# Optimization experiments

Hardware: AMD Instinct MI355X
Metric: run time of the kernel (lower is better)

Reference implementation:

```python
import jax, jax.numpy as jnp
import numpy as np

H, KD, VD, KNN = 8, 64, 64, 128
D, FC, N, S = 512, 2048, 4, 1024
GW_DEC, GW_ENC = 0.5, 0.5
EPS = 1e-5
SCALE = float(np.sqrt(KD))


def _layer_norm(x):
    # nn.LayerNorm(out_dim, eps=1e-5, elementwise_affine=False)
    m = jnp.mean(x, -1, keepdims=True)
    v = jnp.var(x, -1, keepdims=True)
    return (x - m) * jax.lax.rsqrt(v + EPS)


def _mha(x, Wk, bk, Wv, bv, Wo, bo, att_graph, gw, mask, Wq=None, bq=None, q_in=None):
    # x: [N,S,D]; per-head projections stacked: Wk [H,D,Kd], Wv [H,D,Vd]
    key = jnp.einsum('nsd,hdk->hnsk', x, Wk) + bk[:, None, None, :]
    value = jnp.einsum('nsd,hdv->hnsv', x, Wv) + bv[:, None, None, :]
    if q_in is None:
        query = key  # self-attention: query = key (as in the torch code)
    else:
        query = jnp.einsum('nqd,hdk->hnqk', q_in, Wq) + bq[:, None, None, :]
    # broadcast-mul-sum in torch == batched matmul
    att = jnp.einsum('hnqk,hnsk->hnqs', query, key) / SCALE  # [H,N,Q,S]
    if mask:
        qlen, slen = att.shape[-2], att.shape[-1]
        causal = jnp.arange(slen)[None, :] <= jnp.arange(qlen)[:, None]
        att = jnp.where(causal, att, -jnp.inf)
    # knn sparsification: keep top-KNN per row, rest -> -inf (equiv to topk+scatter for distinct values)
    thresh = jax.lax.top_k(att, KNN)[0][..., -1:]
    att = jnp.where(att >= thresh, att, -jnp.inf)
    att = jax.nn.softmax(att, axis=-1)
    # blend with precomputed (softmaxed) graph attention
    att = gw * att_graph + (1.0 - gw) * att
    ctx = jnp.einsum('hnqs,hnsv->hnqv', att, value)  # [H,N,Q,Vd]
    ctx = jnp.transpose(ctx, (1, 2, 0, 3)).reshape(ctx.shape[1], ctx.shape[2], H * VD)
    return ctx @ Wo + bo


def setup_inputs() -> dict:
    key = jax.random.key(0)
    ks = jax.random.split(key, 22)
    p = lambda k, shp: (0.02 * jax.random.normal(k, shp)).astype(jnp.float32)
    return {
        'z': jax.random.normal(ks[0], (N, S, D), jnp.float32),
        'y': jax.random.normal(ks[1], (N, S, D), jnp.float32),
        'graph_dec': jax.random.normal(ks[2], (S, S), jnp.float32),
        'graph_enc': jax.random.normal(ks[3], (S, S), jnp.float32),
        'dec_Wk': p(ks[4], (H, D, KD)), 'dec_bk': p(ks[5], (H, KD)),
        'dec_Wv': p(ks[6], (H, D, VD)), 'dec_bv': p(ks[7], (H, VD)),
        'dec_Wo': p(ks[8], (H * VD, D)), 'dec_bo': p(ks[9], (D,)),
        'enc_Wk': p(ks[10], (H, D, KD)), 'enc_bk': p(ks[11], (H, KD)),
        'enc_Wq': p(ks[12], (H, D, KD)), 'enc_bq': p(ks[13], (H, KD)),
        'enc_Wv': p(ks[14], (H, D, VD)), 'enc_bv': p(ks[15], (H, VD)),
        'enc_Wo': p(ks[16], (H * VD, D)), 'enc_bo': p(ks[17], (D,)),
        'fc_W1': p(ks[18], (D, FC)), 'fc_b1': p(ks[19], (FC,)),
        'fc_W2': p(ks[20], (FC, D)), 'fc_b2': p(ks[21], (D,)),
    }


def reference(z, y, graph_dec, graph_enc, dec_Wk, dec_bk, dec_Wv, dec_bv, dec_Wo, dec_bo, enc_Wk, enc_bk, enc_Wq, enc_bq, enc_Wv, enc_bv, enc_Wo, enc_bo, fc_W1, fc_b1, fc_W2, fc_b2):
    # graphs are row-softmaxed at construction time in the torch module
    gdec = jax.nn.softmax(graph_dec, axis=-1)
    genc = jax.nn.softmax(graph_enc, axis=-1)
    # 1) masked decoder self-attention on y
    h = _mha(y, dec_Wk, dec_bk, dec_Wv, dec_bv, dec_Wo, dec_bo, gdec, GW_DEC, True)
    h = _layer_norm(h + y)
    # 2) encoder-decoder attention: keys/values from z, query from h via query_keys (query_key=True)
    h2 = _mha(z, enc_Wk, enc_bk, enc_Wv, enc_bv, enc_Wo, enc_bo, genc, GW_ENC, False, enc_Wq, enc_bq, h)
    h2 = _layer_norm(h2 + h)
    # 3) two-layer MLP
    h3 = jax.nn.relu(h2 @ fc_W1 + fc_b1) @ fc_W2 + fc_b2
    return _layer_norm(h3 + h2)
```

## Files before the change

kernel.cpp:

```cpp
#include <hip/hip_runtime.h>
#include <stdint.h>

typedef short short8 __attribute__((ext_vector_type(8)));
typedef short short4v __attribute__((ext_vector_type(4)));
typedef float floatx4 __attribute__((ext_vector_type(4)));
typedef unsigned uint4v __attribute__((ext_vector_type(4)));

#define H_  8
#define NB_ 4
#define S_  1024
#define D_  512
#define KD_ 64

__device__ __forceinline__ short f2bf(float f){
    unsigned u = __builtin_bit_cast(unsigned, f);
    u += 0x7fffu + ((u>>16)&1u);
    return (short)(u>>16);
}
__device__ __forceinline__ float wred_addf(float x){
    #pragma unroll
    for(int o=32;o>0;o>>=1) x += __shfl_xor(x,o,64);
    return x;
}
__device__ __forceinline__ float wred_maxf(float x){
    #pragma unroll
    for(int o=32;o>0;o>>=1) x = fmaxf(x,__shfl_xor(x,o,64));
    return x;
}
__device__ __forceinline__ unsigned umaxu(unsigned a, unsigned b){ return a>b?a:b; }
__device__ __forceinline__ unsigned uminu(unsigned a, unsigned b){ return a<b?a:b; }

template<int CTRL, int RMASK, int BC>
__device__ __forceinline__ unsigned dppu(unsigned x){
    return (unsigned)__builtin_amdgcn_update_dpp(0, (int)x, CTRL, RMASK, 0xf, BC);
}
template<int CTRL, int RMASK>
__device__ __forceinline__ unsigned dppu_m1(unsigned x){
    return (unsigned)__builtin_amdgcn_update_dpp((int)0xFFFFFFFF, (int)x, CTRL, RMASK, 0xf, 0);
}
__device__ __forceinline__ unsigned wsum_dpp_u(unsigned x){
    x += dppu<0x111,0xf,1>(x);
    x += dppu<0x112,0xf,1>(x);
    x += dppu<0x114,0xf,1>(x);
    x += dppu<0x118,0xf,1>(x);
    x += dppu<0x142,0xa,0>(x);
    x += dppu<0x143,0xc,0>(x);
    return (unsigned)__builtin_amdgcn_readlane((int)x, 63);
}
__device__ __forceinline__ unsigned wmax_dpp_u(unsigned x){
    x = umaxu(x, dppu<0x111,0xf,1>(x));
    x = umaxu(x, dppu<0x112,0xf,1>(x));
    x = umaxu(x, dppu<0x114,0xf,1>(x));
    x = umaxu(x, dppu<0x118,0xf,1>(x));
    x = umaxu(x, dppu<0x142,0xa,0>(x));
    x = umaxu(x, dppu<0x143,0xc,0>(x));
    return (unsigned)__builtin_amdgcn_readlane((int)x, 63);
}
__device__ __forceinline__ unsigned wmin_dpp_u(unsigned x){
    x = uminu(x, dppu_m1<0x111,0xf>(x));
    x = uminu(x, dppu_m1<0x112,0xf>(x));
    x = uminu(x, dppu_m1<0x114,0xf>(x));
    x = uminu(x, dppu_m1<0x118,0xf>(x));
    x = uminu(x, dppu_m1<0x142,0xa>(x));
    x = uminu(x, dppu_m1<0x143,0xc>(x));
    return (unsigned)__builtin_amdgcn_readlane((int)x, 63);
}
__device__ __forceinline__ float addu_f(float a, unsigned b){
    return a + __builtin_bit_cast(float, b);
}
__device__ __forceinline__ float wsum_dpp_f(float x){
    x = addu_f(x, dppu<0x111,0xf,1>(__builtin_bit_cast(unsigned,x)));
    x = addu_f(x, dppu<0x112,0xf,1>(__builtin_bit_cast(unsigned,x)));
    x = addu_f(x, dppu<0x114,0xf,1>(__builtin_bit_cast(unsigned,x)));
    x = addu_f(x, dppu<0x118,0xf,1>(__builtin_bit_cast(unsigned,x)));
    x = addu_f(x, dppu<0x142,0xa,0>(__builtin_bit_cast(unsigned,x)));
    x = addu_f(x, dppu<0x143,0xc,0>(__builtin_bit_cast(unsigned,x)));
    return __builtin_bit_cast(float, (unsigned)__builtin_amdgcn_readlane((int)__builtin_bit_cast(unsigned, x), 63));
}
__device__ __forceinline__ unsigned cvt_pk_bf16(float a, float b){
    unsigned r;
    asm("v_cvt_pk_bf16_f32 %0, %1, %2" : "=v"(r) : "v"(a), "v"(b));
    return r;
}
__device__ __forceinline__ unsigned count128(const unsigned (&kv)[16], unsigned mid){
    unsigned cv = 0u;
    #pragma unroll
    for(int j=0;j<8;j++) cv += (unsigned)(kv[j] >= mid);
    unsigned cs = 0u;
    #pragma unroll
    for(int j=8;j<16;j++) cs += (unsigned)__popcll(__ballot(kv[j] >= mid));
    return wsum_dpp_u(cv) + cs;
}

__global__ __launch_bounds__(256) void cvt2_kernel(const float* __restrict__ a, const float* __restrict__ b,
                                                   short* __restrict__ oa, short* __restrict__ ob){
    const float* in = blockIdx.y ? b : a;
    short* out = blockIdx.y ? ob : oa;
    int i = (blockIdx.x*256 + threadIdx.x)*4;
    floatx4 v = *(const floatx4*)(in + i);
    short4v r;
    #pragma unroll
    for(int j=0;j<4;j++) r[j] = f2bf(v[j]);
    *(short4v*)(out + i) = r;
}

__global__ __launch_bounds__(256) void wtrans5_kernel(
    const float* __restrict__ dWk, const float* __restrict__ dWv,
    const float* __restrict__ eWk, const float* __restrict__ eWv, const float* __restrict__ eWq,
    short* __restrict__ wKVd, short* __restrict__ wKVe, short* __restrict__ wQet)
{
    __shared__ float t[32][33];
    int zz = blockIdx.z; int w = zz>>3, h = zz&7;
    const float* src; short* dst;
    if(w==0){ src = dWk + h*32768; dst = wKVd + h*65536; }
    else if(w==1){ src = dWv + h*32768; dst = wKVd + h*65536 + 32768; }
    else if(w==2){ src = eWk + h*32768; dst = wKVe + h*65536; }
    else if(w==3){ src = eWv + h*32768; dst = wKVe + h*65536 + 32768; }
    else { src = eWq + h*32768; dst = wQet + h*32768; }
    const int R = 512, C = 64;
    int c0 = blockIdx.x*32, r0 = blockIdx.y*32;
    int tid = threadIdx.x;
    int r = tid>>3, cq = (tid&7)*4;
    #pragma unroll
    for(int i=0;i<4;i++) t[r][cq+i] = src[(r0+r)*C + c0+cq+i];
    __syncthreads();
    int c = tid>>3, rq = (tid&7)*4;
    #pragma unroll
    for(int i=0;i<4;i++) dst[(c0+c)*R + r0+rq+i] = f2bf(t[rq+i][c]);
}

__global__ __launch_bounds__(256) void wtrans4_kernel(
    const float* __restrict__ dWo, const float* __restrict__ eWo,
    const float* __restrict__ W1, const float* __restrict__ W2,
    short* __restrict__ oWod, short* __restrict__ oWoe,
    short* __restrict__ oW1, short* __restrict__ oW2)
{
    __shared__ float t[32][33];
    int id = blockIdx.x;
    const float* src; short* dst; int R, C, c0, r0;
    if(id < 512){
        src = (id<256)? dWo : eWo; dst = (id<256)? oWod : oWoe;
        int tt = id & 255; R = 512; C = 512;
        c0 = (tt&15)*32; r0 = (tt>>4)*32;
    } else if(id < 1536){
        src = W1; dst = oW1; int tt = id - 512; R = 512; C = 2048;
        c0 = (tt&63)*32; r0 = (tt>>6)*32;
    } else {
        src = W2; dst = oW2; int tt = id - 1536; R = 2048; C = 512;
        c0 = (tt&15)*32; r0 = (tt>>4)*32;
    }
    int tid = threadIdx.x;
    int r = tid>>3, cq = (tid&7)*4;
    #pragma unroll
    for(int i=0;i<4;i++) t[r][cq+i] = src[(long)(r0+r)*C + c0+cq+i];
    __syncthreads();
    int c = tid>>3, rq = (tid&7)*4;
    #pragma unroll
    for(int i=0;i<4;i++) dst[(long)(c0+c)*R + r0+rq+i] = f2bf(t[rq+i][c]);
}

__global__ __launch_bounds__(256) void graph_softmax_kernel(const float* __restrict__ g0,
                                                            const float* __restrict__ g1,
                                                            short* __restrict__ o0,
                                                            short* __restrict__ o1){
    int row = blockIdx.x;
    const float* g = blockIdx.y ? g1 : g0;
    short* o = blockIdx.y ? o1 : o0;
    const float* gr = g + (long)row*S_;
    short* orow = o + (long)row*S_;
    int tid = threadIdx.x, wave = tid>>6, lane = tid&63;
    __shared__ float red[8];
    float v[4]; float mx = -3.0e38f;
    #pragma unroll
    for(int i=0;i<4;i++){ v[i] = gr[tid + 256*i]; mx = fmaxf(mx, v[i]); }
    mx = wred_maxf(mx);
    if(lane==0) red[wave] = mx;
    __syncthreads();
    mx = fmaxf(fmaxf(red[0],red[1]), fmaxf(red[2],red[3]));
    float s = 0.f;
    #pragma unroll
    for(int i=0;i<4;i++){ v[i] = __expf(v[i]-mx); s += v[i]; }
    s = wred_addf(s);
    if(lane==0) red[4+wave] = s;
    __syncthreads();
    s = red[4]+red[5]+red[6]+red[7];
    float inv = 0.5f/s;
    #pragma unroll
    for(int i=0;i<4;i++) orow[tid + 256*i] = f2bf(v[i]*inv);
}

template<int KV>
__global__ __launch_bounds__(256) void gemm_proj_kernel(
    const short* __restrict__ A, const short* __restrict__ Bt,
    const float* __restrict__ b1, const float* __restrict__ b2,
    short* __restrict__ o1, short* __restrict__ o2)
{
    constexpr int TN = KV ? 128 : 64;
    constexpr int NI = TN/32;
    __shared__ short As[64*32];
    __shared__ short Bs[TN*32];
    int z = blockIdx.z;
    int m0 = blockIdx.x*64;
    const short* Bb = Bt + (long)z*(TN*512);
    int tid = threadIdx.x, wave = tid>>6, lane = tid&63, quad = lane>>4, nl = lane&15;
    int wm = (wave&1)*32, wn = (wave>>1)*(TN/2);
    floatx4 acc[2][NI];
    #pragma unroll
    for(int i=0;i<2;i++)
        #pragma unroll
        for(int j=0;j<NI;j++) acc[i][j] = (floatx4){0.f,0.f,0.f,0.f};
    int r = tid>>2, c = (tid&3)*8;
    for(int k0=0;k0<512;k0+=32){
        __syncthreads();
        __builtin_amdgcn_global_load_lds(
            (const __attribute__((address_space(1))) unsigned*)(A + (long)(m0 + r)*512 + k0 + c),
            (__attribute__((address_space(3))) unsigned*)((char*)As + wave*1024), 16, 0, 0);
        #pragma unroll
        for(int i=0;i<TN/64;i++)
            __builtin_amdgcn_global_load_lds(
                (const __attribute__((address_space(1))) unsigned*)(Bb + (long)(r + i*64)*512 + k0 + c),
                (__attribute__((address_space(3))) unsigned*)((char*)Bs + i*4096 + wave*1024), 16, 0, 0);
        __syncthreads();
        short8 af[2], bfr[NI];
        #pragma unroll
        for(int i=0;i<2;i++) af[i] = *(const short8*)(As + (wm + i*16 + nl)*32 + quad*8);
        #pragma unroll
        for(int j=0;j<NI;j++) bfr[j] = *(const short8*)(Bs + (wn + j*16 + nl)*32 + quad*8);
        #pragma unroll
        for(int i=0;i<2;i++)
            #pragma unroll
            for(int j=0;j<NI;j++)
                acc[i][j] = __builtin_amdgcn_mfma_f32_16x16x32_bf16(af[i],bfr[j],acc[i][j],0,0,0);
    }
    #pragma unroll
    for(int j=0;j<NI;j++){
        int n = wn + j*16 + nl;
        float bv = (KV && n >= 64) ? b2[z*64 + n - 64] : b1[z*64 + n];
        #pragma unroll
        for(int i=0;i<2;i++){
            #pragma unroll
            for(int rr=0;rr<4;rr++){
                int m = m0 + wm + i*16 + quad*4 + rr;
                float v = acc[i][j][rr] + bv;
                long zb = (long)(z*NB_ + (m>>10));
                if(KV && n >= 64) o2[ (zb*KD_ + (n-64))*S_ + (m&1023) ] = f2bf(v);
                else              o1[ (zb*S_ + (m&1023))*KD_ + n ] = f2bf(v);
            }
        }
    }
}

template<int TM, int TN, int OUTBF, int RELU>
__global__ __launch_bounds__(256) void gemm_big_kernel(
    const short* __restrict__ A, const short* __restrict__ Bt, const float* __restrict__ bias,
    void* __restrict__ out, int M, int N, int K)
{
    __shared__ short As[TM*32];
    __shared__ short Bs[TN*32];
    int m0 = blockIdx.x*TM, n0 = blockIdx.y*TN;
    int tid = threadIdx.x, wave = tid>>6, lane = tid&63, quad = lane>>4, nl = lane&15;
    constexpr int MI = TM/32, NI = TN/32;
    int wm = (wave&1)*(TM/2), wn = (wave>>1)*(TN/2);
    floatx4 acc[MI][NI];
    #pragma unroll
    for(int i=0;i<MI;i++)
        #pragma unroll
        for(int j=0;j<NI;j++) acc[i][j] = (floatx4){0.f,0.f,0.f,0.f};

    int r = tid>>2, c = (tid&3)*8;
    for(int k0=0;k0<K;k0+=32){
        __syncthreads();
        #pragma unroll
        for(int i=0;i<TM/64;i++)
            __builtin_amdgcn_global_load_lds(
                (const __attribute__((address_space(1))) unsigned*)(A + (long)(m0 + r + i*64)*K + k0 + c),
                (__attribute__((address_space(3))) unsigned*)((char*)As + i*4096 + wave*1024),
                16, 0, 0);
        #pragma unroll
        for(int i=0;i<TN/64;i++)
            __builtin_amdgcn_global_load_lds(
                (const __attribute__((address_space(1))) unsigned*)(Bt + (long)(n0 + r + i*64)*K + k0 + c),
                (__attribute__((address_space(3))) unsigned*)((char*)Bs + i*4096 + wave*1024),
                16, 0, 0);
        __syncthreads();
        short8 af[MI], bfr[NI];
        #pragma unroll
        for(int i=0;i<MI;i++) af[i] = *(const short8*)(As + (wm + i*16 + nl)*32 + quad*8);
        #pragma unroll
        for(int j=0;j<NI;j++) bfr[j] = *(const short8*)(Bs + (wn + j*16 + nl)*32 + quad*8);
        #pragma unroll
        for(int i=0;i<MI;i++)
            #pragma unroll
            for(int j=0;j<NI;j++)
                acc[i][j] = __builtin_amdgcn_mfma_f32_16x16x32_bf16(af[i],bfr[j],acc[i][j],0,0,0);
    }
    #pragma unroll
    for(int j=0;j<NI;j++){
        int n = n0 + wn + j*16 + nl;
        float bv = bias[n];
        #pragma unroll
        for(int i=0;i<MI;i++){
            #pragma unroll
            for(int rr=0;rr<4;rr++){
                int m = m0 + wm + i*16 + quad*4 + rr;
                float v = acc[i][j][rr] + bv;
                if(RELU) v = fmaxf(v, 0.f);
                if(OUTBF) ((short*)out)[(long)m*N + n] = f2bf(v);
                else      ((float*)out)[(long)m*N + n] = v;
            }
        }
    }
}

__global__ __launch_bounds__(512,6) void attn_kernel(
    const short* __restrict__ Qb, const short* __restrict__ Kb, const short* __restrict__ Vt,
    const short* __restrict__ graph, short* __restrict__ ctx, int causal)
{
    __shared__ short attb[16*1024];
    __shared__ float pbuf[16*68];
    int hn = blockIdx.x, qt = blockIdx.y;
    int h = hn>>2, n = hn&3;
    int q0 = qt*16;
    int tid=threadIdx.x, wave=tid>>6, lane=tid&63, quad=lane>>4, nl=lane&15;

    if(causal){
        uint4v fv = (uint4v){0xff80ff80u,0xff80ff80u,0xff80ff80u,0xff80ff80u};
        #pragma unroll
        for(int i=0;i<4;i++) *(uint4v*)((char*)attb + tid*16 + i*8192) = fv;
        __syncthreads();
    }

    const short* Qp = Qb + ((long)hn*S_ + q0 + nl)*KD_ + quad*8;
    short8 aq0 = *(const short8*)(Qp);
    short8 aq1 = *(const short8*)(Qp + 32);
    const short* Kp = Kb + (long)hn*S_*KD_;
    int stmax = causal ? qt : 63;
    for(int st=wave; st<=stmax; st+=8){
        const short* kp = Kp + (st*16 + nl)*KD_ + quad*8;
        short8 b0 = *(const short8*)(kp);
        short8 b1 = *(const short8*)(kp + 32);
        floatx4 cc = (floatx4){0.f,0.f,0.f,0.f};
        cc = __builtin_amdgcn_mfma_f32_16x16x32_bf16(aq0,b0,cc,0,0,0);
        cc = __builtin_amdgcn_mfma_f32_16x16x32_bf16(aq1,b1,cc,0,0,0);
        int s = st*16 + nl;
        #pragma unroll
        for(int rr=0;rr<4;rr++){
            int q = quad*4 + rr;
            short val = f2bf(cc[rr]*0.125f);
            if(causal && s > q0 + q) val = (short)0xff80;
            attb[q*1024 + ((s + 8*q)&1023)] = val;
        }
    }
    __syncthreads();

    #pragma unroll 1
    for(int rp=0; rp<2; ++rp){
        int q = wave*2 + rp;
        int qg = q0 + q;
        short* rowp = attb + q*1024;
        int sb = lane*16;
        int p0 = (sb + 8*q) & 1023;
        const short* grow = graph + (long)qg*1024 + sb;
        uint4v g0 = *(const uint4v*)(grow);
        uint4v g1 = *(const uint4v*)(grow + 8);
        uint4v u0 = *(const uint4v*)(rowp + p0);
        uint4v u1 = *(const uint4v*)(rowp + ((p0+8)&1023));
        unsigned pr[8];
        #pragma unroll
        for(int i=0;i<4;i++){ pr[i] = u0[i]; pr[4+i] = u1[i]; }
        unsigned kv[16];
        #pragma unroll
        for(int i=0;i<8;i++){
            unsigned u = pr[i];
            unsigned kp = u ^ (0x80008000u + ((u>>15)&0x00010001u)*0x7fffu);
            kv[2*i]   = kp & 0xffffu;
            kv[2*i+1] = kp >> 16;
        }
        unsigned a0 = umaxu(kv[0],kv[1]),  a1 = umaxu(kv[2],kv[3]);
        unsigned a2 = umaxu(kv[4],kv[5]),  a3 = umaxu(kv[6],kv[7]);
        unsigned a4 = umaxu(kv[8],kv[9]),  a5 = umaxu(kv[10],kv[11]);
        unsigned a6 = umaxu(kv[12],kv[13]),a7 = umaxu(kv[14],kv[15]);
        unsigned mk = umaxu(umaxu(umaxu(a0,a1),umaxu(a2,a3)), umaxu(umaxu(a4,a5),umaxu(a6,a7)));
        unsigned mks = wmax_dpp_u(mk);
        unsigned lmin = wmin_dpp_u(mk);
        unsigned lo, hi;
        {
            unsigned cnt = count128(kv, lmin);
            if(cnt >= 128u){ lo = lmin; hi = (cnt == 128u) ? (lmin + 1u) : (mks + 1u); }
            else           { lo = 0u;   hi = lmin; }
        }
        while(hi - lo > 1u){
            unsigned mid = (lo + hi) >> 1;
            unsigned cnt = count128(kv, mid);
            if(cnt >= 128u){ lo = mid; if(cnt == 128u) break; }
            else hi = mid;
        }
        unsigned uo = (mks & 0x8000u) ? ((mks & 0x7fffu)<<16) : ((~mks)<<16);
        float mxf = __builtin_bit_cast(float, uo);
        float ev[16]; float sm = 0.f;
        #pragma unroll
        for(int i=0;i<8;i++){
            float f0 = __builtin_bit_cast(float, pr[i] << 16);
            float f1 = __builtin_bit_cast(float, pr[i] & 0xffff0000u);
            float e0 = __expf(f0 - mxf);
            float e1 = __expf(f1 - mxf);
            e0 = (kv[2*i]   >= lo) ? e0 : 0.f;
            e1 = (kv[2*i+1] >= lo) ? e1 : 0.f;
            ev[2*i] = e0; ev[2*i+1] = e1;
            sm += e0 + e1;
        }
        sm = wsum_dpp_f(sm);
        float inv = 0.5f / sm;
        uint4v w0, w1;
        #pragma unroll
        for(int i=0;i<4;i++){
            float gl0 = __builtin_bit_cast(float, g0[i] << 16);
            float gh0 = __builtin_bit_cast(float, g0[i] & 0xffff0000u);
            w0[i] = cvt_pk_bf16(fmaf(ev[2*i], inv, gl0), fmaf(ev[2*i+1], inv, gh0));
            float gl1 = __builtin_bit_cast(float, g1[i] << 16);
            float gh1 = __builtin_bit_cast(float, g1[i] & 0xffff0000u);
            w1[i] = cvt_pk_bf16(fmaf(ev[8+2*i], inv, gl1), fmaf(ev[8+2*i+1], inv, gh1));
        }
        *(uint4v*)(rowp + p0) = w0;
        *(uint4v*)(rowp + ((p0+8)&1023)) = w1;
    }
    __syncthreads();

    int vh = wave & 3, sh = wave >> 2;
    int v0 = vh*16;
    const short* Vp = Vt + ((long)hn*KD_ + v0 + nl)*S_;
    floatx4 o4 = (floatx4){0.f,0.f,0.f,0.f};
    int arow = nl;
    int sbase = sh*512;
    for(int s0=sbase; s0<sbase+512; s0+=32){
        int cs = (s0 + quad*8 + 8*arow) & 1023;
        short8 ap = *(const short8*)(attb + arow*1024 + cs);
        short8 bv = *(const short8*)(Vp + s0 + quad*8);
        o4 = __builtin_amdgcn_mfma_f32_16x16x32_bf16(ap,bv,o4,0,0,0);
    }
    if(sh==1){
        #pragma unroll
        for(int rr=0;rr<4;rr++) pbuf[(quad*4+rr)*68 + v0 + nl] = o4[rr];
    }
    __syncthreads();
    if(sh==0){
        #pragma unroll
        for(int rr=0;rr<4;rr++){
            int q = quad*4 + rr;
            float v = o4[rr] + pbuf[q*68 + v0 + nl];
            ctx[ ((long)(n*S_ + q0 + q))*512 + h*KD_ + v0 + nl ] = f2bf(v);
        }
    }
}

__global__ __launch_bounds__(256) void ln_kernel(const float* __restrict__ x, const float* __restrict__ res,
                                                 float* __restrict__ outf, short* __restrict__ outb){
    long row = blockIdx.x;
    const float* xr = x + row*D_;
    const float* rr = res + row*D_;
    int tid = threadIdx.x, wave = tid>>6, lane = tid&63;
    float t0 = xr[tid] + rr[tid];
    float t1 = xr[tid+256] + rr[tid+256];
    float s = t0 + t1, s2 = t0*t0 + t1*t1;
    __shared__ float red[8];
    s = wred_addf(s); s2 = wred_addf(s2);
    if(lane==0){ red[wave] = s; red[4+wave] = s2; }
    __syncthreads();
    s  = red[0]+red[1]+red[2]+red[3];
    s2 = red[4]+red[5]+red[6]+red[7];
    float mean = s*(1.f/512.f);
    float var = s2*(1.f/512.f) - mean*mean;
    float rs = rsqrtf(var + 1e-5f);
    float o0 = (t0-mean)*rs, o1 = (t1-mean)*rs;
    if(outf){ outf[row*D_+tid] = o0; outf[row*D_+tid+256] = o1; }
    if(outb){ outb[row*D_+tid] = f2bf(o0); outb[row*D_+tid+256] = f2bf(o1); }
}

extern "C" void kernel_launch(void* const* d_in, const int* in_sizes, int n_in,
                              void* d_out, int out_size, void* d_ws, size_t ws_size,
                              hipStream_t stream)
{
    const float* z         = (const float*)d_in[0];
    const float* y         = (const float*)d_in[1];
    const float* graph_dec = (const float*)d_in[2];
    const float* graph_enc = (const float*)d_in[3];
    const float* dec_Wk = (const float*)d_in[4];  const float* dec_bk = (const float*)d_in[5];
    const float* dec_Wv = (const float*)d_in[6];  const float* dec_bv = (const float*)d_in[7];
    const float* dec_Wo = (const float*)d_in[8];  const float* dec_bo = (const float*)d_in[9];
    const float* enc_Wk = (const float*)d_in[10]; const float* enc_bk = (const float*)d_in[11];
    const float* enc_Wq = (const float*)d_in[12]; const float* enc_bq = (const float*)d_in[13];
    const float* enc_Wv = (const float*)d_in[14]; const float* enc_bv = (const float*)d_in[15];
    const float* enc_Wo = (const float*)d_in[16]; const float* enc_bo = (const float*)d_in[17];
    const float* fc_W1  = (const float*)d_in[18]; const float* fc_b1  = (const float*)d_in[19];
    const float* fc_W2  = (const float*)d_in[20]; const float* fc_b2  = (const float*)d_in[21];

    char* ws = (char*)d_ws;
    short* gdec  = (short*)(ws + 0x0000000);
    short* genc  = (short*)(ws + 0x0400000);
    short* y_bf  = (short*)(ws + 0x0800000);
    short* z_bf  = (short*)(ws + 0x0C00000);
    short* Kdec  = (short*)(ws + 0x1000000);
    short* Vtdec = (short*)(ws + 0x1400000);
    short* Kenc  = (short*)(ws + 0x1800000);
    short* Vtenc = (short*)(ws + 0x1C00000);
    short* Qenc  = (short*)(ws + 0x2000000);
    short* ctx   = (short*)(ws + 0x2400000);
    float* tmp   = (float*)(ws + 0x2800000);
    float* hbuf  = (float*)(ws + 0x3000000);
    short* h_bf  = (short*)(ws + 0x3800000);
    float* h2    = (float*)(ws + 0x3C00000);
    short* h2_bf = (short*)(ws + 0x4400000);
    short* fc1   = (short*)(ws + 0x4800000);
    short* wKVd  = (short*)(ws + 0x5800000);
    short* wKVe  = (short*)(ws + 0x5900000);
    short* wQet  = (short*)(ws + 0x5A00000);
    short* wOdt  = (short*)(ws + 0x5A80000);
    short* wOet  = (short*)(ws + 0x5B00000);
    short* wF1t  = (short*)(ws + 0x5B80000);
    short* wF2t  = (short*)(ws + 0x5D80000);
    float* outp  = (float*)d_out;

    dim3 B(256);
    wtrans5_kernel<<<dim3(2,16,40),B,0,stream>>>(dec_Wk, dec_Wv, enc_Wk, enc_Wv, enc_Wq, wKVd, wKVe, wQet);
    wtrans4_kernel<<<dim3(2560),B,0,stream>>>(dec_Wo, enc_Wo, fc_W1, fc_W2, wOdt, wOet, wF1t, wF2t);
    cvt2_kernel<<<dim3(2048,2),B,0,stream>>>(y, z, y_bf, z_bf);
    graph_softmax_kernel<<<dim3(1024,2),B,0,stream>>>(graph_dec, graph_enc, gdec, genc);
    gemm_proj_kernel<1><<<dim3(64,1,8),B,0,stream>>>(y_bf, wKVd, dec_bk, dec_bv, Kdec, Vtdec);
    attn_kernel<<<dim3(32,64),dim3(512),0,stream>>>(Kdec, Kdec, Vtdec, gdec, ctx, 1);
    gemm_big_kernel<64,128,0,0><<<dim3(64,4),B,0,stream>>>(ctx, wOdt, dec_bo, tmp, 4096, 512, 512);
    ln_kernel<<<dim3(4096),B,0,stream>>>(tmp, y, hbuf, h_bf);
    gemm_proj_kernel<1><<<dim3(64,1,8),B,0,stream>>>(z_bf, wKVe, enc_bk, enc_bv, Kenc, Vtenc);
    gemm_proj_kernel<0><<<dim3(64,1,8),B,0,stream>>>(h_bf, wQet, enc_bq, (const float*)0, Qenc, (short*)0);
    attn_kernel<<<dim3(32,64),dim3(512),0,stream>>>(Qenc, Kenc, Vtenc, genc, ctx, 0);
    gemm_big_kernel<64,128,0,0><<<dim3(64,4),B,0,stream>>>(ctx, wOet, enc_bo, tmp, 4096, 512, 512);
    ln_kernel<<<dim3(4096),B,0,stream>>>(tmp, hbuf, h2, h2_bf);
    gemm_big_kernel<128,128,1,1><<<dim3(32,16),B,0,stream>>>(h2_bf, wF1t, fc_b1, fc1, 4096, 2048, 512);
    gemm_big_kernel<64,128,0,0><<<dim3(64,4),B,0,stream>>>(fc1, wF2t, fc_b2, tmp, 4096, 512, 2048);
    ln_kernel<<<dim3(4096),B,0,stream>>>(tmp, h2, outp, (short*)0);
}
```

Measured before the change: 387.9 us.

## Fuse prep kernels, merge KV projections, fuse output GEMMs with LayerNorm, interpolate top-k search

Folds the four preprocessing kernels into one prep kernel and merges the decoder and encoder K/V projections into a single launch. The three output-projection GEMMs now do bias, residual add and LayerNorm inside one 16-row by 512-column tile per block, which drops the fp32 tmp buffer and the separate ln_kernel launches. The top-k threshold search in attention now alternates interpolation steps with bisection steps to need fewer count iterations. The trade-off is that the fused GEMM+LN uses small 16-row tiles with 1024 threads and only 256 blocks, so it reuses each B tile less and may run below full occupancy.

```diff
diff --git a/kernel.cpp b/kernel.cpp
--- a/kernel.cpp
+++ b/kernel.cpp
@@ -92,123 +92,125 @@
     return wsum_dpp_u(cv) + cs;
 }
 
-__global__ __launch_bounds__(256) void cvt2_kernel(const float* __restrict__ a, const float* __restrict__ b,
-                                                   short* __restrict__ oa, short* __restrict__ ob){
-    const float* in = blockIdx.y ? b : a;
-    short* out = blockIdx.y ? ob : oa;
-    int i = (blockIdx.x*256 + threadIdx.x)*4;
-    floatx4 v = *(const floatx4*)(in + i);
-    short4v r;
-    #pragma unroll
-    for(int j=0;j<4;j++) r[j] = f2bf(v[j]);
-    *(short4v*)(out + i) = r;
-}
-
-__global__ __launch_bounds__(256) void wtrans5_kernel(
+__global__ __launch_bounds__(256) void prep_kernel(
     const float* __restrict__ dWk, const float* __restrict__ dWv,
     const float* __restrict__ eWk, const float* __restrict__ eWv, const float* __restrict__ eWq,
-    short* __restrict__ wKVd, short* __restrict__ wKVe, short* __restrict__ wQet)
-{
-    __shared__ float t[32][33];
-    int zz = blockIdx.z; int w = zz>>3, h = zz&7;
-    const float* src; short* dst;
-    if(w==0){ src = dWk + h*32768; dst = wKVd + h*65536; }
-    else if(w==1){ src = dWv + h*32768; dst = wKVd + h*65536 + 32768; }
-    else if(w==2){ src = eWk + h*32768; dst = wKVe + h*65536; }
-    else if(w==3){ src = eWv + h*32768; dst = wKVe + h*65536 + 32768; }
-    else { src = eWq + h*32768; dst = wQet + h*32768; }
-    const int R = 512, C = 64;
-    int c0 = blockIdx.x*32, r0 = blockIdx.y*32;
-    int tid = threadIdx.x;
-    int r = tid>>3, cq = (tid&7)*4;
-    #pragma unroll
-    for(int i=0;i<4;i++) t[r][cq+i] = src[(r0+r)*C + c0+cq+i];
-    __syncthreads();
-    int c = tid>>3, rq = (tid&7)*4;
-    #pragma unroll
-    for(int i=0;i<4;i++) dst[(c0+c)*R + r0+rq+i] = f2bf(t[rq+i][c]);
-}
-
-__global__ __launch_bounds__(256) void wtrans4_kernel(
     const float* __restrict__ dWo, const float* __restrict__ eWo,
     const float* __restrict__ W1, const float* __restrict__ W2,
+    const float* __restrict__ y, const float* __restrict__ z,
+    const float* __restrict__ g0, const float* __restrict__ g1,
+    short* __restrict__ wKVd, short* __restrict__ wKVe, short* __restrict__ wQet,
     short* __restrict__ oWod, short* __restrict__ oWoe,
-    short* __restrict__ oW1, short* __restrict__ oW2)
+    short* __restrict__ oW1, short* __restrict__ oW2,
+    short* __restrict__ y_bf, short* __restrict__ z_bf,
+    short* __restrict__ og0, short* __restrict__ og1)
 {
     __shared__ float t[32][33];
     int id = blockIdx.x;
-    const float* src; short* dst; int R, C, c0, r0;
-    if(id < 512){
-        src = (id<256)? dWo : eWo; dst = (id<256)? oWod : oWoe;
-        int tt = id & 255; R = 512; C = 512;
-        c0 = (tt&15)*32; r0 = (tt>>4)*32;
-    } else if(id < 1536){
-        src = W1; dst = oW1; int tt = id - 512; R = 512; C = 2048;
-        c0 = (tt&63)*32; r0 = (tt>>6)*32;
+    int tid = threadIdx.x;
+    if(id < 1280){
+        int zz = id >> 5; int rem = id & 31; int by = rem >> 1, bx = rem & 1;
+        int w = zz>>3, h = zz&7;
+        const float* src; short* dst;
+        if(w==0){ src = dWk + h*32768; dst = wKVd + h*65536; }
+        else if(w==1){ src = dWv + h*32768; dst = wKVd + h*65536 + 32768; }
+        else if(w==2){ src = eWk + h*32768; dst = wKVe + h*65536; }
+        else if(w==3){ src = eWv + h*32768; dst = wKVe + h*65536 + 32768; }
+        else { src = eWq + h*32768; dst = wQet + h*32768; }
+        int c0 = bx*32, r0 = by*32;
+        int r = tid>>3, cq = (tid&7)*4;
+        #pragma unroll
+        for(int i=0;i<4;i++) t[r][cq+i] = src[(r0+r)*64 + c0+cq+i];
+        __syncthreads();
+        int c = tid>>3, rq = (tid&7)*4;
+        #pragma unroll
+        for(int i=0;i<4;i++) dst[(c0+c)*512 + r0+rq+i] = f2bf(t[rq+i][c]);
+    } else if(id < 3840){
+        int id2 = id - 1280;
+        const float* src; short* dst; int R, C, c0, r0;
+        if(id2 < 512){
+            src = (id2<256)? dWo : eWo; dst = (id2<256)? oWod : oWoe;
+            int tt = id2 & 255; R = 512; C = 512;
+            c0 = (tt&15)*32; r0 = (tt>>4)*32;
+        } else if(id2 < 1536){
+            src = W1; dst = oW1; int tt = id2 - 512; R = 512; C = 2048;
+            c0 = (tt&63)*32; r0 = (tt>>6)*32;
+        } else {
+            src = W2; dst = oW2; int tt = id2 - 1536; R = 2048; C = 512;
+            c0 = (tt&15)*32; r0 = (tt>>4)*32;
+        }
+        int r = tid>>3, cq = (tid&7)*4;
+        #pragma unroll
+        for(int i=0;i<4;i++) t[r][cq+i] = src[(long)(r0+r)*C + c0+cq+i];
+        __syncthreads();
+        int c = tid>>3, rq = (tid&7)*4;
+        #pragma unroll
+        for(int i=0;i<4;i++) dst[(long)(c0+c)*R + r0+rq+i] = f2bf(t[rq+i][c]);
+    } else if(id < 7936){
+        int tt = id - 3840;
+        int bx = tt & 2047, by = tt >> 11;
+        const float* in = by ? z : y;
+        short* out = by ? z_bf : y_bf;
+        int i = (bx*256 + tid)*4;
+        floatx4 v = *(const floatx4*)(in + i);
+        short4v r;
+        #pragma unroll
+        for(int j=0;j<4;j++) r[j] = f2bf(v[j]);
+        *(short4v*)(out + i) = r;
     } else {
-        src = W2; dst = oW2; int tt = id - 1536; R = 2048; C = 512;
-        c0 = (tt&15)*32; r0 = (tt>>4)*32;
-    }
-    int tid = threadIdx.x;
-    int r = tid>>3, cq = (tid&7)*4;
-    #pragma unroll
-    for(int i=0;i<4;i++) t[r][cq+i] = src[(long)(r0+r)*C + c0+cq+i];
-    __syncthreads();
-    int c = tid>>3, rq = (tid&7)*4;
-    #pragma unroll
-    for(int i=0;i<4;i++) dst[(long)(c0+c)*R + r0+rq+i] = f2bf(t[rq+i][c]);
-}
-
-__global__ __launch_bounds__(256) void graph_softmax_kernel(const float* __restrict__ g0,
-                                                            const float* __restrict__ g1,
-                                                            short* __restrict__ o0,
-                                                            short* __restrict__ o1){
-    int row = blockIdx.x;
-    const float* g = blockIdx.y ? g1 : g0;
-    short* o = blockIdx.y ? o1 : o0;
-    const float* gr = g + (long)row*S_;
-    short* orow = o + (long)row*S_;
-    int tid = threadIdx.x, wave = tid>>6, lane = tid&63;
-    __shared__ float red[8];
-    float v[4]; float mx = -3.0e38f;
-    #pragma unroll
-    for(int i=0;i<4;i++){ v[i] = gr[tid + 256*i]; mx = fmaxf(mx, v[i]); }
-    mx = wred_maxf(mx);
-    if(lane==0) red[wave] = mx;
-    __syncthreads();
-    mx = fmaxf(fmaxf(red[0],red[1]), fmaxf(red[2],red[3]));
-    float s = 0.f;
-    #pragma unroll
-    for(int i=0;i<4;i++){ v[i] = __expf(v[i]-mx); s += v[i]; }
-    s = wred_addf(s);
-    if(lane==0) red[4+wave] = s;
-    __syncthreads();
-    s = red[4]+red[5]+red[6]+red[7];
-    float inv = 0.5f/s;
-    #pragma unroll
-    for(int i=0;i<4;i++) orow[tid + 256*i] = f2bf(v[i]*inv);
-}
-
-template<int KV>
-__global__ __launch_bounds__(256) void gemm_proj_kernel(
-    const short* __restrict__ A, const short* __restrict__ Bt,
-    const float* __restrict__ b1, const float* __restrict__ b2,
-    short* __restrict__ o1, short* __restrict__ o2)
+        int tt = id - 7936;
+        int row = tt & 1023, by = tt >> 10;
+        const float* g = by ? g1 : g0;
+        short* o = by ? og1 : og0;
+        const float* gr = g + (long)row*S_;
+        short* orow = o + (long)row*S_;
+        int wave = tid>>6, lane = tid&63;
+        float* red = &t[0][0];
+        float v[4]; float mx = -3.0e38f;
+        #pragma unroll
+        for(int i=0;i<4;i++){ v[i] = gr[tid + 256*i]; mx = fmaxf(mx, v[i]); }
+        mx = wred_maxf(mx);
+        if(lane==0) red[wave] = mx;
+        __syncthreads();
+        mx = fmaxf(fmaxf(red[0],red[1]), fmaxf(red[2],red[3]));
+        float s = 0.f;
+        #pragma unroll
+        for(int i=0;i<4;i++){ v[i] = __expf(v[i]-mx); s += v[i]; }
+        s = wred_addf(s);
+        if(lane==0) red[4+wave] = s;
+        __syncthreads();
+        s = red[4]+red[5]+red[6]+red[7];
+        float inv = 0.5f/s;
+        #pragma unroll
+        for(int i=0;i<4;i++) orow[tid + 256*i] = f2bf(v[i]*inv);
+    }
+}
+
+__global__ __launch_bounds__(256) void gemm_projkv_kernel(
+    const short* __restrict__ Ay, const short* __restrict__ Az,
+    const short* __restrict__ Bd, const short* __restrict__ Be,
+    const float* __restrict__ dbk, const float* __restrict__ dbv,
+    const float* __restrict__ ebk, const float* __restrict__ ebv,
+    short* __restrict__ Kd, short* __restrict__ Vd,
+    short* __restrict__ Ke, short* __restrict__ Ve)
 {
-    constexpr int TN = KV ? 128 : 64;
-    constexpr int NI = TN/32;
     __shared__ short As[64*32];
-    __shared__ short Bs[TN*32];
-    int z = blockIdx.z;
+    __shared__ short Bs[128*32];
+    int z = blockIdx.z; int enc = z>>3; int zl = z&7;
+    const short* A  = enc ? Az : Ay;
+    const short* Bb = (enc ? Be : Bd) + zl*65536;
+    const float* b1 = enc ? ebk : dbk;
+    const float* b2 = enc ? ebv : dbv;
+    short* o1 = enc ? Ke : Kd;
+    short* o2 = enc ? Ve : Vd;
     int m0 = blockIdx.x*64;
-    const short* Bb = Bt + (long)z*(TN*512);
     int tid = threadIdx.x, wave = tid>>6, lane = tid&63, quad = lane>>4, nl = lane&15;
-    int wm = (wave&1)*32, wn = (wave>>1)*(TN/2);
-    floatx4 acc[2][NI];
+    int wm = (wave&1)*32, wn = (wave>>1)*64;
+    floatx4 acc[2][4];
     #pragma unroll
     for(int i=0;i<2;i++)
         #pragma unroll
-        for(int j=0;j<NI;j++) acc[i][j] = (floatx4){0.f,0.f,0.f,0.f};
+        for(int j=0;j<4;j++) acc[i][j] = (floatx4){0.f,0.f,0.f,0.f};
     int r = tid>>2, c = (tid&3)*8;
     for(int k0=0;k0<512;k0+=32){
         __syncthreads();
@@ -216,26 +218,81 @@
             (const __attribute__((address_space(1))) unsigned*)(A + (long)(m0 + r)*512 + k0 + c),
             (__attribute__((address_space(3))) unsigned*)((char*)As + wave*1024), 16, 0, 0);
         #pragma unroll
-        for(int i=0;i<TN/64;i++)
+        for(int i=0;i<2;i++)
             __builtin_amdgcn_global_load_lds(
                 (const __attribute__((address_space(1))) unsigned*)(Bb + (long)(r + i*64)*512 + k0 + c),
                 (__attribute__((address_space(3))) unsigned*)((char*)Bs + i*4096 + wave*1024), 16, 0, 0);
         __syncthreads();
-        short8 af[2], bfr[NI];
+        short8 af[2], bfr[4];
         #pragma unroll
         for(int i=0;i<2;i++) af[i] = *(const short8*)(As + (wm + i*16 + nl)*32 + quad*8);
         #pragma unroll
-        for(int j=0;j<NI;j++) bfr[j] = *(const short8*)(Bs + (wn + j*16 + nl)*32 + quad*8);
+        for(int j=0;j<4;j++) bfr[j] = *(const short8*)(Bs + (wn + j*16 + nl)*32 + quad*8);
         #pragma unroll
         for(int i=0;i<2;i++)
             #pragma unroll
-            for(int j=0;j<NI;j++)
+            for(int j=0;j<4;j++)
                 acc[i][j] = __builtin_amdgcn_mfma_f32_16x16x32_bf16(af[i],bfr[j],acc[i][j],0,0,0);
     }
     #pragma unroll
-    for(int j=0;j<NI;j++){
+    for(int j=0;j<4;j++){
         int n = wn + j*16 + nl;
-        float bv = (KV && n >= 64) ? b2[z*64 + n - 64] : b1[z*64 + n];
+        float bv = (n >= 64) ? b2[zl*64 + n - 64] : b1[zl*64 + n];
+        #pragma unroll
+        for(int i=0;i<2;i++){
+            #pragma unroll
+            for(int rr=0;rr<4;rr++){
+                int m = m0 + wm + i*16 + quad*4 + rr;
+                float v = acc[i][j][rr] + bv;
+                long zb = (long)(zl*NB_ + (m>>10));
+                if(n >= 64) o2[ (zb*KD_ + (n-64))*S_ + (m&1023) ] = f2bf(v);
+                else        o1[ (zb*S_ + (m&1023))*KD_ + n ] = f2bf(v);
+            }
+        }
+    }
+}
+
+__global__ __launch_bounds__(256) void gemm_projq_kernel(
+    const short* __restrict__ A, const short* __restrict__ Bt,
+    const float* __restrict__ b1, short* __restrict__ o1)
+{
+    __shared__ short As[64*32];
+    __shared__ short Bs[64*32];
+    int z = blockIdx.z;
+    int m0 = blockIdx.x*64;
+    const short* Bb = Bt + (long)z*(64*512);
+    int tid = threadIdx.x, wave = tid>>6, lane = tid&63, quad = lane>>4, nl = lane&15;
+    int wm = (wave&1)*32, wn = (wave>>1)*32;
+    floatx4 acc[2][2];
+    #pragma unroll
+    for(int i=0;i<2;i++)
+        #pragma unroll
+        for(int j=0;j<2;j++) acc[i][j] = (floatx4){0.f,0.f,0.f,0.f};
+    int r = tid>>2, c = (tid&3)*8;
+    for(int k0=0;k0<512;k0+=32){
+        __syncthreads();
+        __builtin_amdgcn_global_load_lds(
+            (const __attribute__((address_space(1))) unsigned*)(A + (long)(m0 + r)*512 + k0 + c),
+            (__attribute__((address_space(3))) unsigned*)((char*)As + wave*1024), 16, 0, 0);
+        __builtin_amdgcn_global_load_lds(
+            (const __attribute__((address_space(1))) unsigned*)(Bb + (long)r*512 + k0 + c),
+            (__attribute__((address_space(3))) unsigned*)((char*)Bs + wave*1024), 16, 0, 0);
+        __syncthreads();
+        short8 af[2], bfr[2];
+        #pragma unroll
+        for(int i=0;i<2;i++) af[i] = *(const short8*)(As + (wm + i*16 + nl)*32 + quad*8);
+        #pragma unroll
+        for(int j=0;j<2;j++) bfr[j] = *(const short8*)(Bs + (wn + j*16 + nl)*32 + quad*8);
+        #pragma unroll
+        for(int i=0;i<2;i++)
+            #pragma unroll
+            for(int j=0;j<2;j++)
+                acc[i][j] = __builtin_amdgcn_mfma_f32_16x16x32_bf16(af[i],bfr[j],acc[i][j],0,0,0);
+    }
+    #pragma unroll
+    for(int j=0;j<2;j++){
+        int n = wn + j*16 + nl;
+        float bv = b1[z*64 + n];
         #pragma unroll
         for(int i=0;i<2;i++){
             #pragma unroll
@@ -243,8 +300,7 @@
                 int m = m0 + wm + i*16 + quad*4 + rr;
                 float v = acc[i][j][rr] + bv;
                 long zb = (long)(z*NB_ + (m>>10));
-                if(KV && n >= 64) o2[ (zb*KD_ + (n-64))*S_ + (m&1023) ] = f2bf(v);
-                else              o1[ (zb*S_ + (m&1023))*KD_ + n ] = f2bf(v);
+                o1[ (zb*S_ + (m&1023))*KD_ + n ] = f2bf(v);
             }
         }
     }
@@ -308,6 +364,87 @@
                 if(OUTBF) ((short*)out)[(long)m*N + n] = f2bf(v);
                 else      ((float*)out)[(long)m*N + n] = v;
             }
+        }
+    }
+}
+
+template<int OUTB>
+__global__ __launch_bounds__(1024) void gemm_ln_kernel(
+    const short* __restrict__ A, const short* __restrict__ Bt,
+    const float* __restrict__ bias, const float* __restrict__ res,
+    float* __restrict__ outf, short* __restrict__ outb, int K)
+{
+    __shared__ short As[16*32];
+    __shared__ short Bs[512*32];
+    __shared__ float redn[2][16][16];
+    int m0 = blockIdx.x*16;
+    int tid = threadIdx.x, wave = tid>>6, lane = tid&63, quad = lane>>4, nl = lane&15;
+    int wn = wave*32;
+    floatx4 acc[2];
+    acc[0] = (floatx4){0.f,0.f,0.f,0.f};
+    acc[1] = (floatx4){0.f,0.f,0.f,0.f};
+    int r = tid>>2, c = (tid&3)*8;
+    for(int k0=0;k0<K;k0+=32){
+        __syncthreads();
+        if(wave==0)
+            __builtin_amdgcn_global_load_lds(
+                (const __attribute__((address_space(1))) unsigned*)(A + (long)(m0 + (lane>>2))*K + k0 + (lane&3)*8),
+                (__attribute__((address_space(3))) unsigned*)((char*)As), 16, 0, 0);
+        #pragma unroll
+        for(int i=0;i<2;i++)
+            __builtin_amdgcn_global_load_lds(
+                (const __attribute__((address_space(1))) unsigned*)(Bt + (long)(r + i*256)*K + k0 + c),
+                (__attribute__((address_space(3))) unsigned*)((char*)Bs + i*16384 + wave*1024), 16, 0, 0);
+        __syncthreads();
+        short8 af = *(const short8*)(As + nl*32 + quad*8);
+        short8 b0 = *(const short8*)(Bs + (wn + nl)*32 + quad*8);
+        short8 b1 = *(const short8*)(Bs + (wn + 16 + nl)*32 + quad*8);
+        acc[0] = __builtin_amdgcn_mfma_f32_16x16x32_bf16(af,b0,acc[0],0,0,0);
+        acc[1] = __builtin_amdgcn_mfma_f32_16x16x32_bf16(af,b1,acc[1],0,0,0);
+    }
+    float t[2][4];
+    #pragma unroll
+    for(int j=0;j<2;j++){
+        int n = wn + j*16 + nl;
+        float bv = bias[n];
+        #pragma unroll
+        for(int rr=0;rr<4;rr++){
+            int m = quad*4 + rr;
+            t[j][rr] = acc[j][rr] + bv + res[(long)(m0+m)*512 + n];
+        }
+    }
+    #pragma unroll
+    for(int rr=0;rr<4;rr++){
+        float s  = t[0][rr] + t[1][rr];
+        float s2 = t[0][rr]*t[0][rr] + t[1][rr]*t[1][rr];
+        #pragma unroll
+        for(int o=1;o<16;o<<=1){ s += __shfl_xor(s,o,16); s2 += __shfl_xor(s2,o,16); }
+        if(nl==0){
+            redn[0][quad*4+rr][wave] = s;
+            redn[1][quad*4+rr][wave] = s2;
+        }
+    }
+    __syncthreads();
+    #pragma unroll
+    for(int rr=0;rr<4;rr++){
+        int row = quad*4 + rr;
+        float s = 0.f, s2 = 0.f;
+        #pragma unroll
+        for(int b=0;b<4;b++){
+            floatx4 p  = *(const floatx4*)&redn[0][row][b*4];
+            floatx4 p2 = *(const floatx4*)&redn[1][row][b*4];
+            s  += p[0]+p[1]+p[2]+p[3];
+            s2 += p2[0]+p2[1]+p2[2]+p2[3];
+        }
+        float mean = s*(1.f/512.f);
+        float var = s2*(1.f/512.f) - mean*mean;
+        float rs = rsqrtf(var + 1e-5f);
+        #pragma unroll
+        for(int j=0;j<2;j++){
+            int n = wn + j*16 + nl;
+            float o = (t[j][rr] - mean)*rs;
+            outf[(long)(m0+row)*512 + n] = o;
+            if(OUTB) outb[(long)(m0+row)*512 + n] = f2bf(o);
         }
     }
 }
@@ -383,17 +520,32 @@
         unsigned mk = umaxu(umaxu(umaxu(a0,a1),umaxu(a2,a3)), umaxu(umaxu(a4,a5),umaxu(a6,a7)));
         unsigned mks = wmax_dpp_u(mk);
         unsigned lmin = wmin_dpp_u(mk);
-        unsigned lo, hi;
+        unsigned lo, hi, clo, chi;
         {
             unsigned cnt = count128(kv, lmin);
-            if(cnt >= 128u){ lo = lmin; hi = (cnt == 128u) ? (lmin + 1u) : (mks + 1u); }
-            else           { lo = 0u;   hi = lmin; }
-        }
+            if(cnt >= 128u){
+                lo = lmin; clo = cnt;
+                hi = (cnt == 128u) ? (lmin + 1u) : (mks + 1u); chi = 0u;
+            } else {
+                lo = 0u; clo = 1024u; hi = lmin; chi = cnt;
+            }
+        }
+        int it = 0;
         while(hi - lo > 1u){
-            unsigned mid = (lo + hi) >> 1;
+            unsigned span = hi - lo;
+            unsigned mid;
+            if((it++ & 1) == 0){
+                float fr = (float)(clo - 128u) / (float)(clo - chi);
+                unsigned off = (unsigned)(fr * (float)span);
+                off = off < 1u ? 1u : off;
+                off = off > span - 1u ? span - 1u : off;
+                mid = lo + off;
+            } else {
+                mid = lo + (span >> 1);
+            }
             unsigned cnt = count128(kv, mid);
-            if(cnt >= 128u){ lo = mid; if(cnt == 128u) break; }
-            else hi = mid;
+            if(cnt >= 128u){ lo = mid; clo = cnt; if(cnt == 128u) break; }
+            else { hi = mid; chi = cnt; }
         }
         unsigned uo = (mks & 0x8000u) ? ((mks & 0x7fffu)<<16) : ((~mks)<<16);
         float mxf = __builtin_bit_cast(float, uo);
@@ -451,29 +603,6 @@
             ctx[ ((long)(n*S_ + q0 + q))*512 + h*KD_ + v0 + nl ] = f2bf(v);
         }
     }
-}
-
-__global__ __launch_bounds__(256) void ln_kernel(const float* __restrict__ x, const float* __restrict__ res,
-                                                 float* __restrict__ outf, short* __restrict__ outb){
-    long row = blockIdx.x;
-    const float* xr = x + row*D_;
-    const float* rr = res + row*D_;
-    int tid = threadIdx.x, wave = tid>>6, lane = tid&63;
-    float t0 = xr[tid] + rr[tid];
-    float t1 = xr[tid+256] + rr[tid+256];
-    float s = t0 + t1, s2 = t0*t0 + t1*t1;
-    __shared__ float red[8];
-    s = wred_addf(s); s2 = wred_addf(s2);
-    if(lane==0){ red[wave] = s; red[4+wave] = s2; }
-    __syncthreads();
-    s  = red[0]+red[1]+red[2]+red[3];
-    s2 = red[4]+red[5]+red[6]+red[7];
-    float mean = s*(1.f/512.f);
-    float var = s2*(1.f/512.f) - mean*mean;
-    float rs = rsqrtf(var + 1e-5f);
-    float o0 = (t0-mean)*rs, o1 = (t1-mean)*rs;
-    if(outf){ outf[row*D_+tid] = o0; outf[row*D_+tid+256] = o1; }
-    if(outb){ outb[row*D_+tid] = f2bf(o0); outb[row*D_+tid+256] = f2bf(o1); }
 }
 
 extern "C" void kernel_launch(void* const* d_in, const int* in_sizes, int n_in,
@@ -505,7 +634,6 @@
     short* Vtenc = (short*)(ws + 0x1C00000);
     short* Qenc  = (short*)(ws + 0x2000000);
     short* ctx   = (short*)(ws + 0x2400000);
-    float* tmp   = (float*)(ws + 0x2800000);
     float* hbuf  = (float*)(ws + 0x3000000);
     short* h_bf  = (short*)(ws + 0x3800000);
     float* h2    = (float*)(ws + 0x3C00000);
@@ -520,21 +648,18 @@
     short* wF2t  = (short*)(ws + 0x5D80000);
     float* outp  = (float*)d_out;
 
-    dim3 B(256);
-    wtrans5_kernel<<<dim3(2,16,40),B,0,stream>>>(dec_Wk, dec_Wv, enc_Wk, enc_Wv, enc_Wq, wKVd, wKVe, wQet);
-    wtrans4_kernel<<<dim3(2560),B,0,stream>>>(dec_Wo, enc_Wo, fc_W1, fc_W2, wOdt, wOet, wF1t, wF2t);
-    cvt2_kernel<<<dim3(2048,2),B,0,stream>>>(y, z, y_bf, z_bf);
-    graph_softmax_kernel<<<dim3(1024,2),B,0,stream>>>(graph_dec, graph_enc, gdec, genc);
-    gemm_proj_kernel<1><<<dim3(64,1,8),B,0,stream>>>(y_bf, wKVd, dec_bk, dec_bv, Kdec, Vtdec);
+    prep_kernel<<<dim3(9984),dim3(256),0,stream>>>(
+        dec_Wk, dec_Wv, enc_Wk, enc_Wv, enc_Wq, dec_Wo, enc_Wo, fc_W1, fc_W2,
+        y, z, graph_dec, graph_enc,
+        wKVd, wKVe, wQet, wOdt, wOet, wF1t, wF2t, y_bf, z_bf, gdec, genc);
+    gemm_projkv_kernel<<<dim3(64,1,16),dim3(256),0,stream>>>(
+        y_bf, z_bf, wKVd, wKVe, dec_bk, dec_bv, enc_bk, enc_bv,
+        Kdec, Vtdec, Kenc, Vtenc);
     attn_kernel<<<dim3(32,64),dim3(512),0,stream>>>(Kdec, Kdec, Vtdec, gdec, ctx, 1);
-    gemm_big_kernel<64,128,0,0><<<dim3(64,4),B,0,stream>>>(ctx, wOdt, dec_bo, tmp, 4096, 512, 512);
-    ln_kernel<<<dim3(4096),B,0,stream>>>(tmp, y, hbuf, h_bf);
-    gemm_proj_kernel<1><<<dim3(64,1,8),B,0,stream>>>(z_bf, wKVe, enc_bk, enc_bv, Kenc, Vtenc);
-    gemm_proj_kernel<0><<<dim3(64,1,8),B,0,stream>>>(h_bf, wQet, enc_bq, (const float*)0, Qenc, (short*)0);
+    gemm_ln_kernel<1><<<dim3(256),dim3(1024),0,stream>>>(ctx, wOdt, dec_bo, y, hbuf, h_bf, 512);
+    gemm_projq_kernel<<<dim3(64,1,8),dim3(256),0,stream>>>(h_bf, wQet, enc_bq, Qenc);
     attn_kernel<<<dim3(32,64),dim3(512),0,stream>>>(Qenc, Kenc, Vtenc, genc, ctx, 0);
-    gemm_big_kernel<64,128,0,0><<<dim3(64,4),B,0,stream>>>(ctx, wOet, enc_bo, tmp, 4096, 512, 512);
-    ln_kernel<<<dim3(4096),B,0,stream>>>(tmp, hbuf, h2, h2_bf);
-    gemm_big_kernel<128,128,1,1><<<dim3(32,16),B,0,stream>>>(h2_bf, wF1t, fc_b1, fc1, 4096, 2048, 512);
-    gemm_big_kernel<64,128,0,0><<<dim3(64,4),B,0,stream>>>(fc1, wF2t, fc_b2, tmp, 4096, 512, 2048);
-    ln_kernel<<<dim3(4096),B,0,stream>>>(tmp, h2, outp, (short*)0);
-}
+    gemm_ln_kernel<1><<<dim3(256),dim3(1024),0,stream>>>(ctx, wOet, enc_bo, hbuf, h2, h2_bf, 512);
+    gemm_big_kernel<128,128,1,1><<<dim3(32,16),dim3(256),0,stream>>>(h2_bf, wF1t, fc_b1, fc1, 4096, 2048, 512);
+    gemm_ln_kernel<0><<<dim3(256),dim3(1024),0,stream>>>(fc1, wF2t, fc_b2, h2, outp, (short*)0, 2048);
+}
```

Result: slower. 417.6 us (+7.7%).
